# Performance work log

Measured on AMD Instinct MI355X. Metric: run time of the kernel, lower is better.

The kernel has to match this reference:

```python
import jax, jax.numpy as jnp
import numpy as np

K = 1024
D = 256
BETA = 0.25


def setup_inputs() -> dict:
    key = jax.random.key(0)
    kx, kc = jax.random.split(key)
    x = jax.random.normal(kx, (64, 32, 32, D), dtype=jnp.float32)
    limit = 1.0 / K
    codebook = jax.random.uniform(kc, (K, D), dtype=jnp.float32, minval=-limit, maxval=limit)
    return {"x": x, "codebook": codebook}


def reference(x, codebook):
    flat = x.reshape(-1, D)                                   # [N, D]
    x2 = jnp.sum(jnp.square(flat), axis=1, keepdims=True)     # [N, 1]
    e2 = jnp.sum(jnp.square(codebook), axis=1)                # [K]
    sim = flat @ codebook.T                                   # [N, K]
    dist = x2 + e2 - 2.0 * sim                                # [N, K]
    idx = jnp.argmin(dist, axis=1)                            # [N]
    q = codebook[idx].reshape(x.shape)                        # [..., D]

    q_st = jax.lax.stop_gradient(q)
    x_st = jax.lax.stop_gradient(x)
    commit = jnp.mean(jnp.square(q_st - x))
    codebk = jnp.mean(jnp.square(q - x_st))
    loss = BETA * commit + codebk

    # code-usage statistics via histogram (equivalent to mean of one-hot)
    counts = jnp.zeros((K,), dtype=x.dtype).at[idx].add(1.0)
    probs = counts / flat.shape[0]
    eps = jnp.asarray(1e-10, dtype=x.dtype)
    H = -jnp.sum(probs * jnp.log2(probs + eps))               # bits/index
    perplexity = jnp.exp(H * jnp.log(jnp.asarray(2.0, dtype=x.dtype)))
    usage = jnp.sum((probs > 0).astype(x.dtype)) / float(K)

    y = x + jax.lax.stop_gradient(q - x)                      # straight-through
    return y, idx, loss, perplexity, usage, H
```

## Files before the change

### kernel.cpp

```cpp
#include <hip/hip_runtime.h>
#include <math.h>

#define D       256
#define KCODES  1024
#define NROWS   65536
#define BETA    0.25f
#define MARGIN  1e-3f
#define MAXSURV 7

typedef __attribute__((ext_vector_type(8))) short bf16x8;
typedef __attribute__((ext_vector_type(4))) float f32x4;

__device__ __forceinline__ unsigned int bf16_rne(float f) {
    unsigned int u = __float_as_uint(f);
    return (u + 0x7FFFu + ((u >> 16) & 1u)) >> 16;
}
__device__ __forceinline__ f32x4 mfma16(bf16x8 a, bf16x8 b, f32x4 c) {
    return __builtin_amdgcn_mfma_f32_16x16x32_bf16(a, b, c, 0, 0, 0);
}

__global__ __launch_bounds__(256) void split_cb_kernel(const float* __restrict__ cb,
                                                       ushort* __restrict__ cs,
                                                       float* __restrict__ e2f) {
    int code = blockIdx.x * 4 + (threadIdx.x >> 6);
    int lane = threadIdx.x & 63;
    float4 v = ((const float4*)(cb + (size_t)code * D))[lane];
    double s = (double)v.x * v.x + (double)v.y * v.y +
               (double)v.z * v.z + (double)v.w * v.w;
    ushort* ph = cs + (size_t)code * 256 + lane * 4;
    ph[0] = (ushort)bf16_rne(v.x); ph[1] = (ushort)bf16_rne(v.y);
    ph[2] = (ushort)bf16_rne(v.z); ph[3] = (ushort)bf16_rne(v.w);
    #pragma unroll
    for (int off = 32; off > 0; off >>= 1) s += __shfl_down(s, off, 64);
    if (lane == 0) e2f[code] = (float)s;
}

__global__ __launch_bounds__(512, 4) void screen_kernel(
    const float* __restrict__ x, const ushort* __restrict__ cs,
    const float* __restrict__ e2f, const float* __restrict__ cb,
    float* __restrict__ out_idxf, unsigned int* __restrict__ counts,
    float* __restrict__ y, float* __restrict__ msepart)
{
    __shared__ __attribute__((aligned(16))) ushort Bt[2][32 * 264];
    __shared__ float x2s[128];
    unsigned* mrg = (unsigned*)&Bt[0][0];
    #define MRG(r, j) mrg[(r) * 33 + (j)]

    const int tid  = threadIdx.x;
    const int wave = tid >> 6, lane = tid & 63;
    const int quad = lane >> 4, m = lane & 15;
    const int rowBase = blockIdx.x * 128;
    const int wrb = rowBase + wave * 16;

    const int sc = tid & 31, sp = tid >> 5;
    bf16x8 stg[2];
    {
        const ushort* src = cs + (size_t)sc * 256 + sp * 16;
        stg[0] = *(const bf16x8*)&src[0];
        stg[1] = *(const bf16x8*)&src[8];
    }

    bf16x8 af[8];
    {
        const float* xr = x + (size_t)(wrb + m) * D;
        double s = 0.0;
        #pragma unroll
        for (int c = 0; c < 8; ++c) {
            float4 f0 = *(const float4*)&xr[c * 32 + quad * 8];
            float4 f1 = *(const float4*)&xr[c * 32 + quad * 8 + 4];
            s += (double)f0.x * f0.x + (double)f0.y * f0.y +
                 (double)f0.z * f0.z + (double)f0.w * f0.w;
            s += (double)f1.x * f1.x + (double)f1.y * f1.y +
                 (double)f1.z * f1.z + (double)f1.w * f1.w;
            float ff[8] = {f0.x, f0.y, f0.z, f0.w, f1.x, f1.y, f1.z, f1.w};
            #pragma unroll
            for (int j = 0; j < 8; ++j) af[c][j] = (short)bf16_rne(ff[j]);
        }
        s += __shfl_xor(s, 16, 64);
        s += __shfl_xor(s, 32, 64);
        if (quad == 0) x2s[wave * 16 + m] = (float)s;
    }

    unsigned u1[4], u2[4];
    #pragma unroll
    for (int r = 0; r < 4; ++r) { u1[r] = 0xFFFFFFFFu; u2[r] = 0xFFFFFFFFu; }

    for (int kt = 0; kt < KCODES / 32; ++kt) {
        {
            ushort* dst = &Bt[kt & 1][sc * 264 + sp * 16];
            *(bf16x8*)&dst[0] = stg[0];
            *(bf16x8*)&dst[8] = stg[1];
        }
        __syncthreads();
        if (kt < KCODES / 32 - 1) {
            const ushort* src = cs + (size_t)((kt + 1) * 32 + sc) * 256 + sp * 16;
            stg[0] = *(const bf16x8*)&src[0];
            stg[1] = *(const bf16x8*)&src[8];
        }

        float e2pa = e2f[kt * 32 + m] + 0.5f;
        float e2pb = e2f[kt * 32 + 16 + m] + 0.5f;

        const ushort* Bcur = &Bt[kt & 1][0];
        #pragma unroll
        for (int nt = 0; nt < 2; ++nt) {
            f32x4 acc = {0.f, 0.f, 0.f, 0.f};
            const ushort* bp = Bcur + (nt * 16 + m) * 264 + quad * 8;
            __builtin_amdgcn_s_setprio(1);
            #pragma unroll
            for (int c = 0; c < 8; ++c) {
                bf16x8 bh = *(const bf16x8*)&bp[c * 32];
                acc = mfma16(af[c], bh, acc);
            }
            __builtin_amdgcn_s_setprio(0);
            unsigned kcode = kt * 32 + nt * 16 + m;
            float e2p = nt ? e2pb : e2pa;
            #pragma unroll
            for (int r = 0; r < 4; ++r) {
                float d = fmaf(-2.f, acc[r], e2p);
                unsigned u = (__float_as_uint(d) & 0xFFFFFC00u) | kcode;
                bool lt1 = u < u1[r];
                bool lt2 = u < u2[r];
                u2[r] = lt2 ? (lt1 ? u1[r] : u) : u2[r];
                u1[r] = lt1 ? u : u1[r];
            }
        }
    }

    #pragma unroll
    for (int r = 0; r < 4; ++r) {
        int rowloc = wave * 16 + quad * 4 + r;
        MRG(rowloc, m * 2 + 0) = u1[r];
        MRG(rowloc, m * 2 + 1) = u2[r];
    }
    __syncthreads();
    if (tid < 128) {
        unsigned umin = 0xFFFFFFFFu;
        #pragma unroll
        for (int j = 0; j < 32; ++j) umin = min(umin, MRG(tid, j));
        float dfloor = __uint_as_float(umin & 0xFFFFFC00u);
        unsigned limu = (__float_as_uint(dfloor + MARGIN) & 0xFFFFFC00u) | 1023u;
        ushort out[8] = {0, 0, 0, 0, 0, 0, 0, 0};
        int cnt = 0;
        for (int j = 0; j < 32; ++j) {
            unsigned u = MRG(tid, j);
            if (u <= limu && cnt < MAXSURV) { out[1 + cnt] = (ushort)(u & 1023u); ++cnt; }
        }
        out[0] = (ushort)cnt;
        *(bf16x8*)&mrg[tid * 33] = *(bf16x8*)out;
    }
    __syncthreads();

    #pragma unroll 2
    for (int i = 0; i < 16; ++i) {
        int rl  = wave * 16 + i;
        int row = rowBase + rl;
        const ushort* lst = (const ushort*)&mrg[rl * 33];
        int cnt = lst[0];
        float4 xv = ((const float4*)(x + (size_t)row * D))[lane];

        int bk;
        if (cnt == 1) {
            bk = lst[1];
        } else {
            float x2 = x2s[rl];
            float bestd = 1e30f;
            int   bestk = 0;
            for (int s = 0; s < cnt; ++s) {
                int k = lst[1 + s];
                float4 cv = ((const float4*)(cb + (size_t)k * D))[lane];
                double p = (double)xv.x * cv.x + (double)xv.y * cv.y +
                           (double)xv.z * cv.z + (double)xv.w * cv.w;
                #pragma unroll
                for (int off = 32; off > 0; off >>= 1) p += __shfl_down(p, off, 64);
                float simf = (float)p;
                float tt   = x2 + e2f[k];
                float dq   = tt - 2.0f * simf;
                if (dq < bestd || (dq == bestd && k < bestk)) { bestd = dq; bestk = k; }
            }
            bk = __shfl(bestk, 0, 64);
        }
        if (lane == 0) {
            out_idxf[row] = (float)bk;
            atomicAdd(&counts[bk], 1u);
        }
        float4 q = ((const float4*)(cb + (size_t)bk * D))[lane];
        float4 dv;
        dv.x = q.x - xv.x; dv.y = q.y - xv.y; dv.z = q.z - xv.z; dv.w = q.w - xv.w;
        float4 yv;
        yv.x = xv.x + dv.x; yv.y = xv.y + dv.y; yv.z = xv.z + dv.z; yv.w = xv.w + dv.w;
        ((float4*)(y + (size_t)row * D))[lane] = yv;
        float s = dv.x * dv.x + dv.y * dv.y + dv.z * dv.z + dv.w * dv.w;
        #pragma unroll
        for (int off = 32; off > 0; off >>= 1) s += __shfl_down(s, off, 64);
        if (lane == 0) msepart[row] = s;
    }
    #undef MRG
}

__global__ __launch_bounds__(1024) void stats_kernel(
    const unsigned int* __restrict__ counts, const float* __restrict__ msepart,
    float* __restrict__ outs)
{
    int t = threadIdx.x;
    float ms = 0.f;
    #pragma unroll
    for (int j = 0; j < 64; ++j) ms += msepart[t + 1024 * j];

    float p = (float)counts[t] * (1.0f / 65536.0f);
    float h = -p * log2f(p + 1e-10f);
    float u = (p > 0.f) ? 1.f : 0.f;
    #pragma unroll
    for (int off = 32; off > 0; off >>= 1) {
        h  += __shfl_down(h,  off, 64);
        u  += __shfl_down(u,  off, 64);
        ms += __shfl_down(ms, off, 64);
    }
    __shared__ float hs[16], us[16], mss[16];
    int lane = t & 63, w = t >> 6;
    if (lane == 0) { hs[w] = h; us[w] = u; mss[w] = ms; }
    __syncthreads();
    if (t == 0) {
        float H = 0.f, U = 0.f, M = 0.f;
        #pragma unroll
        for (int i = 0; i < 16; ++i) { H += hs[i]; U += us[i]; M += mss[i]; }
        float m = M * (1.0f / 16777216.0f);
        float loss = BETA * m + m;
        float perp = expf(H * 0.69314718055994530942f);
        outs[0] = loss;
        outs[1] = perp;
        outs[2] = U * (1.0f / 1024.0f);
        outs[3] = H;
    }
}

extern "C" void kernel_launch(void* const* d_in, const int* in_sizes, int n_in,
                              void* d_out, int out_size, void* d_ws, size_t ws_size,
                              hipStream_t stream) {
    const float* x  = (const float*)d_in[0];
    const float* cb = (const float*)d_in[1];
    float* out      = (float*)d_out;

    float* y        = out;
    float* out_idxf = out + 16777216;
    float* outs     = out + 16777216 + 65536;

    float*        e2f     = (float*)((char*)d_ws + 262144);
    unsigned int* counts  = (unsigned int*)((char*)d_ws + 266240);
    ushort*       cs      = (ushort*)((char*)d_ws + 1318976);
    float*        msepart = (float*)((char*)d_ws + 1843264);

    hipMemsetAsync((char*)d_ws + 266240, 0, 4096, stream);
    split_cb_kernel<<<KCODES / 4, 256, 0, stream>>>(cb, cs, e2f);
    screen_kernel<<<NROWS / 128, 512, 0, stream>>>(x, cs, e2f, cb,
                                                   out_idxf, counts, y, msepart);
    stats_kernel<<<1, 1024, 0, stream>>>(counts, msepart, outs);
}
```

Before: 191.9 us.

## Double rows per wave, prefetch two codebook tiles per sync, fold memset into split kernel

```diff
diff --git a/kernel.cpp b/kernel.cpp
--- a/kernel.cpp
+++ b/kernel.cpp
@@ -21,7 +21,9 @@
 
 __global__ __launch_bounds__(256) void split_cb_kernel(const float* __restrict__ cb,
                                                        ushort* __restrict__ cs,
-                                                       float* __restrict__ e2f) {
+                                                       float* __restrict__ e2f,
+                                                       unsigned int* __restrict__ counts) {
+    if (threadIdx.x < 4) counts[blockIdx.x * 4 + threadIdx.x] = 0u;
     int code = blockIdx.x * 4 + (threadIdx.x >> 6);
     int lane = threadIdx.x & 63;
     float4 v = ((const float4*)(cb + (size_t)code * D))[lane];
@@ -35,34 +37,39 @@
     if (lane == 0) e2f[code] = (float)s;
 }
 
-__global__ __launch_bounds__(512, 4) void screen_kernel(
+__global__ __launch_bounds__(512) void screen_kernel(
     const float* __restrict__ x, const ushort* __restrict__ cs,
     const float* __restrict__ e2f, const float* __restrict__ cb,
     float* __restrict__ out_idxf, unsigned int* __restrict__ counts,
     float* __restrict__ y, float* __restrict__ msepart)
 {
-    __shared__ __attribute__((aligned(16))) ushort Bt[2][32 * 264];
-    __shared__ float x2s[128];
+    __shared__ __attribute__((aligned(16))) ushort Bt[4][32 * 264];
+    __shared__ float x2s[256];
     unsigned* mrg = (unsigned*)&Bt[0][0];
     #define MRG(r, j) mrg[(r) * 33 + (j)]
 
     const int tid  = threadIdx.x;
     const int wave = tid >> 6, lane = tid & 63;
     const int quad = lane >> 4, m = lane & 15;
-    const int rowBase = blockIdx.x * 128;
-    const int wrb = rowBase + wave * 16;
+    const int rowBase = blockIdx.x * 256;
+    const int wrb = rowBase + wave * 32;
 
     const int sc = tid & 31, sp = tid >> 5;
-    bf16x8 stg[2];
+
+    bf16x8 stg[4];
     {
-        const ushort* src = cs + (size_t)sc * 256 + sp * 16;
-        stg[0] = *(const bf16x8*)&src[0];
-        stg[1] = *(const bf16x8*)&src[8];
-    }
-
-    bf16x8 af[8];
-    {
-        const float* xr = x + (size_t)(wrb + m) * D;
+        const ushort* s0 = cs + (size_t)sc * 256 + sp * 16;
+        const ushort* s1 = cs + (size_t)(32 + sc) * 256 + sp * 16;
+        stg[0] = *(const bf16x8*)&s0[0];
+        stg[1] = *(const bf16x8*)&s0[8];
+        stg[2] = *(const bf16x8*)&s1[0];
+        stg[3] = *(const bf16x8*)&s1[8];
+    }
+
+    bf16x8 af[2][8];
+    #pragma unroll
+    for (int t = 0; t < 2; ++t) {
+        const float* xr = x + (size_t)(wrb + t * 16 + m) * D;
         double s = 0.0;
         #pragma unroll
         for (int c = 0; c < 8; ++c) {
@@ -74,76 +81,108 @@
                  (double)f1.z * f1.z + (double)f1.w * f1.w;
             float ff[8] = {f0.x, f0.y, f0.z, f0.w, f1.x, f1.y, f1.z, f1.w};
             #pragma unroll
-            for (int j = 0; j < 8; ++j) af[c][j] = (short)bf16_rne(ff[j]);
+            for (int j = 0; j < 8; ++j) af[t][c][j] = (short)bf16_rne(ff[j]);
         }
         s += __shfl_xor(s, 16, 64);
         s += __shfl_xor(s, 32, 64);
-        if (quad == 0) x2s[wave * 16 + m] = (float)s;
-    }
-
-    unsigned u1[4], u2[4];
-    #pragma unroll
-    for (int r = 0; r < 4; ++r) { u1[r] = 0xFFFFFFFFu; u2[r] = 0xFFFFFFFFu; }
-
-    for (int kt = 0; kt < KCODES / 32; ++kt) {
-        {
-            ushort* dst = &Bt[kt & 1][sc * 264 + sp * 16];
-            *(bf16x8*)&dst[0] = stg[0];
-            *(bf16x8*)&dst[8] = stg[1];
+        if (quad == 0) x2s[wave * 32 + t * 16 + m] = (float)s;
+    }
+
+    {
+        ushort* d0 = &Bt[0][sc * 264 + sp * 16];
+        ushort* d1 = &Bt[1][sc * 264 + sp * 16];
+        *(bf16x8*)&d0[0] = stg[0]; *(bf16x8*)&d0[8] = stg[1];
+        *(bf16x8*)&d1[0] = stg[2]; *(bf16x8*)&d1[8] = stg[3];
+    }
+    {
+        const ushort* s2 = cs + (size_t)(64 + sc) * 256 + sp * 16;
+        const ushort* s3 = cs + (size_t)(96 + sc) * 256 + sp * 16;
+        stg[0] = *(const bf16x8*)&s2[0];
+        stg[1] = *(const bf16x8*)&s2[8];
+        stg[2] = *(const bf16x8*)&s3[0];
+        stg[3] = *(const bf16x8*)&s3[8];
+    }
+
+    unsigned u1[2][4], u2[2][4];
+    #pragma unroll
+    for (int t = 0; t < 2; ++t)
+        #pragma unroll
+        for (int r = 0; r < 4; ++r) { u1[t][r] = 0xFFFFFFFFu; u2[t][r] = 0xFFFFFFFFu; }
+
+    __syncthreads();
+
+    for (int j = 0; j < 16; ++j) {
+        #pragma unroll
+        for (int h = 0; h < 2; ++h) {
+            const int kt = 2 * j + h;
+            const ushort* Bcur = &Bt[kt & 3][0];
+            float e2pa = e2f[kt * 32 + m] + 0.5f;
+            float e2pb = e2f[kt * 32 + 16 + m] + 0.5f;
+            #pragma unroll
+            for (int nt = 0; nt < 2; ++nt) {
+                f32x4 acc0 = {0.f, 0.f, 0.f, 0.f};
+                f32x4 acc1 = {0.f, 0.f, 0.f, 0.f};
+                const ushort* bp = Bcur + (nt * 16 + m) * 264 + quad * 8;
+                __builtin_amdgcn_s_setprio(1);
+                #pragma unroll
+                for (int c = 0; c < 8; ++c) {
+                    bf16x8 bh = *(const bf16x8*)&bp[c * 32];
+                    acc0 = mfma16(af[0][c], bh, acc0);
+                    acc1 = mfma16(af[1][c], bh, acc1);
+                }
+                __builtin_amdgcn_s_setprio(0);
+                unsigned kcode = kt * 32 + nt * 16 + m;
+                float e2p = nt ? e2pb : e2pa;
+                #pragma unroll
+                for (int t = 0; t < 2; ++t) {
+                    f32x4 acc = t ? acc1 : acc0;
+                    #pragma unroll
+                    for (int r = 0; r < 4; ++r) {
+                        float d = fmaf(-2.f, acc[r], e2p);
+                        unsigned u = (__float_as_uint(d) & 0xFFFFFC00u) | kcode;
+                        u2[t][r] = min(max(u, u1[t][r]), u2[t][r]);
+                        u1[t][r] = min(u, u1[t][r]);
+                    }
+                }
+            }
+        }
+        if (j < 15) {
+            const int ta = 2 * j + 2, tb = 2 * j + 3;
+            ushort* da = &Bt[ta & 3][sc * 264 + sp * 16];
+            ushort* db = &Bt[tb & 3][sc * 264 + sp * 16];
+            *(bf16x8*)&da[0] = stg[0]; *(bf16x8*)&da[8] = stg[1];
+            *(bf16x8*)&db[0] = stg[2]; *(bf16x8*)&db[8] = stg[3];
+            if (j < 14) {
+                const ushort* sa = cs + (size_t)((ta + 2) * 32 + sc) * 256 + sp * 16;
+                const ushort* sb = cs + (size_t)((tb + 2) * 32 + sc) * 256 + sp * 16;
+                stg[0] = *(const bf16x8*)&sa[0];
+                stg[1] = *(const bf16x8*)&sa[8];
+                stg[2] = *(const bf16x8*)&sb[0];
+                stg[3] = *(const bf16x8*)&sb[8];
+            }
         }
         __syncthreads();
-        if (kt < KCODES / 32 - 1) {
-            const ushort* src = cs + (size_t)((kt + 1) * 32 + sc) * 256 + sp * 16;
-            stg[0] = *(const bf16x8*)&src[0];
-            stg[1] = *(const bf16x8*)&src[8];
-        }
-
-        float e2pa = e2f[kt * 32 + m] + 0.5f;
-        float e2pb = e2f[kt * 32 + 16 + m] + 0.5f;
-
-        const ushort* Bcur = &Bt[kt & 1][0];
-        #pragma unroll
-        for (int nt = 0; nt < 2; ++nt) {
-            f32x4 acc = {0.f, 0.f, 0.f, 0.f};
-            const ushort* bp = Bcur + (nt * 16 + m) * 264 + quad * 8;
-            __builtin_amdgcn_s_setprio(1);
-            #pragma unroll
-            for (int c = 0; c < 8; ++c) {
-                bf16x8 bh = *(const bf16x8*)&bp[c * 32];
-                acc = mfma16(af[c], bh, acc);
-            }
-            __builtin_amdgcn_s_setprio(0);
-            unsigned kcode = kt * 32 + nt * 16 + m;
-            float e2p = nt ? e2pb : e2pa;
-            #pragma unroll
-            for (int r = 0; r < 4; ++r) {
-                float d = fmaf(-2.f, acc[r], e2p);
-                unsigned u = (__float_as_uint(d) & 0xFFFFFC00u) | kcode;
-                bool lt1 = u < u1[r];
-                bool lt2 = u < u2[r];
-                u2[r] = lt2 ? (lt1 ? u1[r] : u) : u2[r];
-                u1[r] = lt1 ? u : u1[r];
-            }
-        }
-    }
-
-    #pragma unroll
-    for (int r = 0; r < 4; ++r) {
-        int rowloc = wave * 16 + quad * 4 + r;
-        MRG(rowloc, m * 2 + 0) = u1[r];
-        MRG(rowloc, m * 2 + 1) = u2[r];
-    }
-    __syncthreads();
-    if (tid < 128) {
+    }
+
+    #pragma unroll
+    for (int t = 0; t < 2; ++t)
+        #pragma unroll
+        for (int r = 0; r < 4; ++r) {
+            int rowloc = wave * 32 + t * 16 + quad * 4 + r;
+            MRG(rowloc, m * 2 + 0) = u1[t][r];
+            MRG(rowloc, m * 2 + 1) = u2[t][r];
+        }
+    __syncthreads();
+    if (tid < 256) {
         unsigned umin = 0xFFFFFFFFu;
         #pragma unroll
-        for (int j = 0; j < 32; ++j) umin = min(umin, MRG(tid, j));
+        for (int jj = 0; jj < 32; ++jj) umin = min(umin, MRG(tid, jj));
         float dfloor = __uint_as_float(umin & 0xFFFFFC00u);
         unsigned limu = (__float_as_uint(dfloor + MARGIN) & 0xFFFFFC00u) | 1023u;
         ushort out[8] = {0, 0, 0, 0, 0, 0, 0, 0};
         int cnt = 0;
-        for (int j = 0; j < 32; ++j) {
-            unsigned u = MRG(tid, j);
+        for (int jj = 0; jj < 32; ++jj) {
+            unsigned u = MRG(tid, jj);
             if (u <= limu && cnt < MAXSURV) { out[1 + cnt] = (ushort)(u & 1023u); ++cnt; }
         }
         out[0] = (ushort)cnt;
@@ -152,8 +191,8 @@
     __syncthreads();
 
     #pragma unroll 2
-    for (int i = 0; i < 16; ++i) {
-        int rl  = wave * 16 + i;
+    for (int i = 0; i < 32; ++i) {
+        int rl  = wave * 32 + i;
         int row = rowBase + rl;
         const ushort* lst = (const ushort*)&mrg[rl * 33];
         int cnt = lst[0];
@@ -250,9 +289,8 @@
     ushort*       cs      = (ushort*)((char*)d_ws + 1318976);
     float*        msepart = (float*)((char*)d_ws + 1843264);
 
-    hipMemsetAsync((char*)d_ws + 266240, 0, 4096, stream);
-    split_cb_kernel<<<KCODES / 4, 256, 0, stream>>>(cb, cs, e2f);
-    screen_kernel<<<NROWS / 128, 512, 0, stream>>>(x, cs, e2f, cb,
+    split_cb_kernel<<<KCODES / 4, 256, 0, stream>>>(cb, cs, e2f, counts);
+    screen_kernel<<<NROWS / 256, 512, 0, stream>>>(x, cs, e2f, cb,
                                                    out_idxf, counts, y, msepart);
     stats_kernel<<<1, 1024, 0, stream>>>(counts, msepart, outs);
 }
```

Result: slower. 197.2 us (+2.8%).
